# Optimization experiments

Hardware: AMD Instinct MI355X
Metric: run time of the kernel (lower is better)

## Reference

```python
import jax, jax.numpy as jnp
import numpy as np

N, M, D = 8192, 8192, 128

def setup_inputs() -> dict:
    key = jax.random.key(0)
    kq, kk, kv = jax.random.split(key, 3)
    Q = jax.random.normal(kq, (N, D), dtype=jnp.float32)
    K = jax.random.normal(kk, (M, D), dtype=jnp.float32)
    V = jax.random.normal(kv, (M, D), dtype=jnp.float32)
    return {"Q": Q, "K": K, "V": V}

def reference(Q, K, V):
    # scores: [N, M], unscaled QK^T
    scores = Q @ K.T
    # NOTE: original uses torch.softmax(scores, dim=0, dtype=float) -> softmax over the
    # QUERY axis (axis 0), normalizing each key-column across queries.
    attn = jax.nn.softmax(scores.astype(jnp.float32), axis=0)
    return attn @ V  # [N, D]
```

## Files before the change

### kernel.cpp

```cpp
#include <hip/hip_runtime.h>
#include <hip/hip_bf16.h>
#include <math.h>

constexpr int N = 8192, M = 8192, D = 128;
constexpr int NE = N * D;
constexpr float SHIFT = 60.0f;
constexpr float LOG2E = 1.4426950408889634f;
constexpr float S2 = 86.56170245333781f;
constexpr int SN_A = 16;
constexpr int PC_KS = 8;
constexpr int MK = M / 32;

typedef unsigned short u16;
typedef unsigned int u32;
using short8 = __attribute__((ext_vector_type(8))) short;
using f32x4  = __attribute__((ext_vector_type(4))) float;

#define MFMA16(a, b, c) __builtin_amdgcn_mfma_f32_16x16x32_bf16((a), (b), (c), 0, 0, 0)

#if __has_builtin(__builtin_amdgcn_exp2f)
#define EXP2(x) __builtin_amdgcn_exp2f(x)
#else
#define EXP2(x) __expf((x) * 0.6931471805599453f)
#endif

constexpr int PR = 40;
constexpr int CP = 136;
constexpr int KP = 136;
constexpr int WP = 72;
constexpr int PP = 72;

__device__ __forceinline__ u16 f2bf_rn(float x) {
  unsigned int u = __float_as_uint(x);
  return (u16)((u + 0x7fffu + ((u >> 16) & 1u)) >> 16);
}
__device__ __forceinline__ float bf2f(u16 h) { return __uint_as_float((unsigned)h << 16); }

__device__ __forceinline__ size_t qk_frag(int rowblk, int kblk, int lane) {
  return (((size_t)rowblk * 4 + kblk) * 64 + lane) * 8;
}
__device__ __forceinline__ size_t pw_frag(int blk16, int mkblk, int lane) {
  return (((size_t)blk16 * MK + mkblk) * 64 + lane) * 8;
}

__global__ __launch_bounds__(256) void convert_frag2(const float4* __restrict__ Qs,
                                                     const float4* __restrict__ Ks,
                                                     u16* __restrict__ Qhi, u16* __restrict__ Qlo,
                                                     u16* __restrict__ Khi, u16* __restrict__ Klo,
                                                     float* __restrict__ colsum) {
  __shared__ u16 LH[64 * CP];
  __shared__ u16 LL[64 * CP];
  const int tid = threadIdx.x;
  const bool isK = blockIdx.y != 0;
  const float4* src = isK ? Ks : Qs;
  u16* hi = isK ? Khi : Qhi;
  u16* lo = isK ? Klo : Qlo;
  const float sc = isK ? 1.0f : LOG2E;
  const int row0 = blockIdx.x * 64;

  if (blockIdx.x == 0 && !isK) {
#pragma unroll
    for (int k = 0; k < M / 256; ++k) colsum[tid + k * 256] = 0.f;
  }

#pragma unroll
  for (int it = 0; it < 8; ++it) {
    int idx = tid + it * 256;
    int rr = idx >> 5, g = idx & 31;
    float4 f = src[(size_t)(row0 + rr) * 32 + g];
    float v[4] = {f.x, f.y, f.z, f.w};
    u16 h[4], l4[4];
#pragma unroll
    for (int j = 0; j < 4; ++j) {
      float x = v[j] * sc;
      h[j] = f2bf_rn(x);
      l4[j] = f2bf_rn(x - bf2f(h[j]));
    }
    u32* ph = (u32*)(LH + rr * CP + g * 4);
    u32* pl = (u32*)(LL + rr * CP + g * 4);
    ph[0] = (u32)h[0] | ((u32)h[1] << 16);
    ph[1] = (u32)h[2] | ((u32)h[3] << 16);
    pl[0] = (u32)l4[0] | ((u32)l4[1] << 16);
    pl[1] = (u32)l4[2] | ((u32)l4[3] << 16);
  }
  __syncthreads();

#pragma unroll
  for (int it = 0; it < 4; ++it) {
    int idx = tid + it * 256;
    int tau = idx >> 6, l = idx & 63;
    int rowblk = tau >> 2, kblk = tau & 3;
    int d = kblk * 32 + (l >> 4) * 8;
    int nl;
    if (isK) {
      nl = ((rowblk >> 1) << 5) + ((l & 15) << 1) + (rowblk & 1);
    } else {
      nl = rowblk * 16 + (l & 15);
    }
    size_t off = qk_frag((row0 >> 4) + rowblk, kblk, l);
    *(short8*)(hi + off) = *(const short8*)(LH + nl * CP + d);
    *(short8*)(lo + off) = *(const short8*)(LL + nl * CP + d);
  }
}

__global__ __launch_bounds__(256, 4) void pass_a_frag(const u16* __restrict__ Qh,
                                                      const u16* __restrict__ Ql,
                                                      const u16* __restrict__ Kh,
                                                      const u16* __restrict__ Kl,
                                                      float* __restrict__ colsum,
                                                      u16* __restrict__ Pf) {
  __shared__ u16 PW[4][2][32 * PR];
  const int tid = threadIdx.x;
  const int w = tid >> 6, lane = tid & 63;
  const int r = lane & 15, q = lane >> 4;
  const int cbase = blockIdx.x * 128 + 32 * w;
  const int mymk = blockIdx.x * 4 + w;
  const int n0 = blockIdx.y * (N / SN_A);

  short8 kh[4][2], kl[4][2];
#pragma unroll
  for (int kk = 0; kk < 4; ++kk)
#pragma unroll
    for (int c = 0; c < 2; ++c) {
      size_t off = qk_frag((cbase >> 4) + c, kk, lane);
      kh[kk][c] = *(const short8*)(Kh + off);
      kl[kk][c] = *(const short8*)(Kl + off);
    }

  float csum[2] = {0.f, 0.f};

#pragma unroll 2
  for (int s = 0; s < (N / SN_A) / 32; ++s) {
    const int nb = n0 + s * 32;
    u16* pw = PW[w][s & 1];
    u32* pwD = (u32*)pw;

    f32x4 acc[2][2];
#pragma unroll
    for (int t = 0; t < 2; ++t)
#pragma unroll
      for (int c = 0; c < 2; ++c) acc[t][c] = (f32x4){-S2, -S2, -S2, -S2};

#pragma unroll
    for (int kk = 0; kk < 4; ++kk) {
      short8 ah[2], al[2];
#pragma unroll
      for (int t = 0; t < 2; ++t) {
        size_t off = qk_frag((nb >> 4) + t, kk, lane);
        ah[t] = *(const short8*)(Qh + off);
        al[t] = *(const short8*)(Ql + off);
      }
#pragma unroll
      for (int t = 0; t < 2; ++t)
#pragma unroll
        for (int c = 0; c < 2; ++c) {
          acc[t][c] = MFMA16(ah[t], kh[kk][c], acc[t][c]);
          acc[t][c] = MFMA16(al[t], kh[kk][c], acc[t][c]);
          acc[t][c] = MFMA16(ah[t], kl[kk][c], acc[t][c]);
        }
    }

#pragma unroll
    for (int t = 0; t < 2; ++t)
#pragma unroll
      for (int rg = 0; rg < 4; ++rg) {
        float e0 = EXP2(acc[t][0][rg]);
        float e1 = EXP2(acc[t][1][rg]);
        csum[0] += e0;
        csum[1] += e1;
        u32 pk = (u32)f2bf_rn(e0) | ((u32)f2bf_rn(e1) << 16);
        pwD[(16 * t + 4 * q + rg) * (PR / 2) + r] = pk;
      }
#pragma unroll
    for (int t = 0; t < 2; ++t) {
      short8 v = *(const short8*)(pw + (16 * t + r) * PR + q * 8);
      *(short8*)(Pf + pw_frag((nb >> 4) + t, mymk, lane)) = v;
    }
  }

  csum[0] += __shfl_xor(csum[0], 16);
  csum[0] += __shfl_xor(csum[0], 32);
  csum[1] += __shfl_xor(csum[1], 16);
  csum[1] += __shfl_xor(csum[1], 32);
  if (lane < 16) {
    atomicAdd(&colsum[cbase + 2 * lane], csum[0]);
    atomicAdd(&colsum[cbase + 2 * lane + 1], csum[1]);
  }
}

__global__ __launch_bounds__(256) void scale_transpose_frag(const float* __restrict__ V,
                                                            const float* __restrict__ colsum,
                                                            u16* __restrict__ Wf) {
  __shared__ float Vs[64][132];
  __shared__ float rls[64];
  const int tid = threadIdx.x;
  const int m0 = blockIdx.x * 64;
#pragma unroll
  for (int it = 0; it < 8; ++it) {
    int idx = tid + it * 256;
    int rr = idx >> 5, g = idx & 31;
    float4 v = *(const float4*)(V + (size_t)(m0 + rr) * D + g * 4);
    Vs[rr][g * 4 + 0] = v.x; Vs[rr][g * 4 + 1] = v.y;
    Vs[rr][g * 4 + 2] = v.z; Vs[rr][g * 4 + 3] = v.w;
  }
  if (tid < 64) rls[tid] = 1.0f / colsum[m0 + tid];
  __syncthreads();
#pragma unroll
  for (int it = 0; it < 4; ++it) {
    int idx = tid + it * 256;
    int dd = idx >> 3, g = idx & 7;
    short8 o;
#pragma unroll
    for (int j = 0; j < 8; ++j) {
      int mm = g * 8 + j;
      o[j] = (short)f2bf_rn(Vs[mm][dd] * rls[mm]);
    }
    *(short8*)(Wf + pw_frag(dd >> 4, (m0 >> 5) + (g >> 2), (dd & 15) + ((g & 3) << 4))) = o;
  }
}

template <bool ATOMIC>
__global__ __launch_bounds__(256, 4) void pass_c_kern(const u16* __restrict__ Pf,
                                                      const u16* __restrict__ Wf,
                                                      float* __restrict__ dst) {
  const int tid = threadIdx.x;
  const int w = tid >> 6, lane = tid & 63;
  const int r = lane & 15, q = lane >> 4;
  const int nblk0 = blockIdx.x * 8 + w * 2;
  const int mk0 = blockIdx.y * (MK / PC_KS);
  constexpr int CNT = MK / PC_KS;

  f32x4 acc[2][8];
#pragma unroll
  for (int i = 0; i < 2; ++i)
#pragma unroll
    for (int dt = 0; dt < 8; ++dt) acc[i][dt] = (f32x4){0.f, 0.f, 0.f, 0.f};

  short8 c0 = *(const short8*)(Pf + pw_frag(nblk0 + 0, mk0, lane));
  short8 c1 = *(const short8*)(Pf + pw_frag(nblk0 + 1, mk0, lane));
  short8 x0 = *(const short8*)(Pf + pw_frag(nblk0 + 0, mk0 + 1, lane));
  short8 x1 = *(const short8*)(Pf + pw_frag(nblk0 + 1, mk0 + 1, lane));

  for (int mk = 0; mk < CNT; ++mk) {
    const int mkg = mk0 + mk;
    const int mk2 = mk + 2 < CNT ? mkg + 2 : mk0;
    short8 p0 = *(const short8*)(Pf + pw_frag(nblk0 + 0, mk2, lane));
    short8 p1 = *(const short8*)(Pf + pw_frag(nblk0 + 1, mk2, lane));
#pragma unroll
    for (int dt = 0; dt < 8; ++dt) {
      short8 b = *(const short8*)(Wf + pw_frag(dt, mkg, lane));
      acc[0][dt] = MFMA16(c0, b, acc[0][dt]);
      acc[1][dt] = MFMA16(c1, b, acc[1][dt]);
    }
    c0 = x0; c1 = x1; x0 = p0; x1 = p1;
  }

  if (ATOMIC) {
#pragma unroll
    for (int i = 0; i < 2; ++i)
#pragma unroll
      for (int dt = 0; dt < 8; ++dt)
#pragma unroll
        for (int rg = 0; rg < 4; ++rg)
          atomicAdd(&dst[(size_t)((nblk0 + i) * 16 + q * 4 + rg) * D + dt * 16 + r],
                    acc[i][dt][rg]);
  } else {
    float* part = dst + (size_t)blockIdx.y * NE;
#pragma unroll
    for (int i = 0; i < 2; ++i)
#pragma unroll
      for (int dt = 0; dt < 8; ++dt)
#pragma unroll
        for (int rg = 0; rg < 4; ++rg)
          part[(size_t)((nblk0 + i) * 16 + q * 4 + rg) * D + dt * 16 + r] = acc[i][dt][rg];
  }
}

__global__ __launch_bounds__(256) void reduce_out(const float4* __restrict__ part,
                                                  float4* __restrict__ out) {
  int i = blockIdx.x * 256 + threadIdx.x;
  float4 s = part[i];
#pragma unroll
  for (int k = 1; k < PC_KS; ++k) {
    float4 p = part[(size_t)k * (NE / 4) + i];
    s.x += p.x; s.y += p.y; s.z += p.z; s.w += p.w;
  }
  out[i] = s;
}

__global__ __launch_bounds__(256) void convert_hilo2(const float4* __restrict__ Qs,
                                                     const float4* __restrict__ Ks,
                                                     ushort4* __restrict__ Qhi, ushort4* __restrict__ Qlo,
                                                     ushort4* __restrict__ Khi, ushort4* __restrict__ Klo) {
  int i = blockIdx.x * 256 + threadIdx.x;
  const float4* src = blockIdx.y ? Ks : Qs;
  ushort4* hi = blockIdx.y ? Khi : Qhi;
  ushort4* lo = blockIdx.y ? Klo : Qlo;
  float4 f = src[i];
  float v[4] = {f.x, f.y, f.z, f.w};
  u16 hs[4], ls[4];
#pragma unroll
  for (int j = 0; j < 4; ++j) {
    hs[j] = f2bf_rn(v[j]);
    ls[j] = f2bf_rn(v[j] - bf2f(hs[j]));
  }
  hi[i] = make_ushort4(hs[0], hs[1], hs[2], hs[3]);
  lo[i] = make_ushort4(ls[0], ls[1], ls[2], ls[3]);
}

__global__ __launch_bounds__(256, 4) void pass_a_fb(const u16* __restrict__ Qh,
                                                    const u16* __restrict__ Ql,
                                                    const u16* __restrict__ Kh,
                                                    const u16* __restrict__ Kl,
                                                    float* __restrict__ colsum) {
  const int tid = threadIdx.x;
  const int w = tid >> 6, lane = tid & 63;
  const int r = lane & 15, q = lane >> 4;
  const int cbase = blockIdx.x * 128 + 32 * w;
  const int n0 = blockIdx.y * (N / 16);

  short8 kh[4][2], kl[4][2];
#pragma unroll
  for (int kk = 0; kk < 4; ++kk)
#pragma unroll
    for (int c = 0; c < 2; ++c) {
      kh[kk][c] = *(const short8*)(Kh + (size_t)(cbase + 16 * c + r) * D + kk * 32 + q * 8);
      kl[kk][c] = *(const short8*)(Kl + (size_t)(cbase + 16 * c + r) * D + kk * 32 + q * 8);
    }

  float csum[2] = {0.f, 0.f};
  for (int s = 0; s < 16; ++s) {
    const int nb = n0 + s * 32;
    f32x4 acc[2][2];
#pragma unroll
    for (int t = 0; t < 2; ++t)
#pragma unroll
      for (int c = 0; c < 2; ++c) acc[t][c] = (f32x4){0.f, 0.f, 0.f, 0.f};
#pragma unroll
    for (int kk = 0; kk < 4; ++kk) {
      short8 ah[2], al[2];
#pragma unroll
      for (int t = 0; t < 2; ++t) {
        ah[t] = *(const short8*)(Qh + (size_t)(nb + t * 16 + r) * D + kk * 32 + q * 8);
        al[t] = *(const short8*)(Ql + (size_t)(nb + t * 16 + r) * D + kk * 32 + q * 8);
      }
#pragma unroll
      for (int t = 0; t < 2; ++t)
#pragma unroll
        for (int c = 0; c < 2; ++c) {
          acc[t][c] = MFMA16(ah[t], kh[kk][c], acc[t][c]);
          acc[t][c] = MFMA16(al[t], kh[kk][c], acc[t][c]);
          acc[t][c] = MFMA16(ah[t], kl[kk][c], acc[t][c]);
        }
    }
#pragma unroll
    for (int t = 0; t < 2; ++t)
#pragma unroll
      for (int c = 0; c < 2; ++c)
#pragma unroll
        for (int rg = 0; rg < 4; ++rg) csum[c] += __expf(acc[t][c][rg] - SHIFT);
  }
  csum[0] += __shfl_xor(csum[0], 16);
  csum[0] += __shfl_xor(csum[0], 32);
  csum[1] += __shfl_xor(csum[1], 16);
  csum[1] += __shfl_xor(csum[1], 32);
  if (lane < 16) {
    atomicAdd(&colsum[cbase + r], csum[0]);
    atomicAdd(&colsum[cbase + 16 + r], csum[1]);
  }
}

__global__ __launch_bounds__(256) void scale_transpose_fb(const float* __restrict__ V,
                                                          const float* __restrict__ colsum,
                                                          u16* __restrict__ Wt) {
  __shared__ float Vs[64][132];
  __shared__ float rls[64];
  const int tid = threadIdx.x;
  const int m0 = blockIdx.x * 64;
#pragma unroll
  for (int it = 0; it < 8; ++it) {
    int idx = tid + it * 256;
    int rr = idx >> 5, g = idx & 31;
    float4 v = *(const float4*)(V + (size_t)(m0 + rr) * D + g * 4);
    Vs[rr][g * 4 + 0] = v.x; Vs[rr][g * 4 + 1] = v.y;
    Vs[rr][g * 4 + 2] = v.z; Vs[rr][g * 4 + 3] = v.w;
  }
  if (tid < 64) rls[tid] = 1.0f / colsum[m0 + tid];
  __syncthreads();
#pragma unroll
  for (int it = 0; it < 4; ++it) {
    int idx = tid + it * 256;
    int dd = idx >> 3, g = idx & 7;
    short8 o;
#pragma unroll
    for (int j = 0; j < 8; ++j) {
      int mm = g * 8 + j;
      o[j] = (short)f2bf_rn(Vs[mm][dd] * rls[mm]);
    }
    *(short8*)(Wt + (size_t)dd * M + m0 + g * 8) = o;
  }
}

__global__ __launch_bounds__(256, 2) void pass_c_fb(const u16* __restrict__ Qh,
                                                    const u16* __restrict__ Ql,
                                                    const u16* __restrict__ Kh,
                                                    const u16* __restrict__ Kl,
                                                    const u16* __restrict__ Wt,
                                                    float* __restrict__ out) {
  __shared__ u16 KsH[64 * KP];
  __shared__ u16 KsL[64 * KP];
  __shared__ u16 Ws[128 * WP];
  __shared__ u16 Ps[4][16 * PP];
  const int tid = threadIdx.x;
  const int w = tid >> 6, lane = tid & 63;
  const int r = lane & 15, q = lane >> 4;
  const size_t nrow = (size_t)blockIdx.x * 64 + w * 16 + r;
  const int mbase = blockIdx.y * (M / 4);

  short8 qh[4], ql[4];
#pragma unroll
  for (int kk = 0; kk < 4; ++kk) {
    qh[kk] = *(const short8*)(Qh + nrow * D + kk * 32 + q * 8);
    ql[kk] = *(const short8*)(Ql + nrow * D + kk * 32 + q * 8);
  }

  f32x4 oacc[8];
#pragma unroll
  for (int dt = 0; dt < 8; ++dt) oacc[dt] = (f32x4){0.f, 0.f, 0.f, 0.f};

  for (int mt = 0; mt < (M / 4) / 64; ++mt) {
    const int m0 = mbase + mt * 64;
    __syncthreads();
#pragma unroll
    for (int it = 0; it < 4; ++it) {
      int idx = tid + it * 256;
      int rr = idx >> 4, g = idx & 15;
      *(short8*)(KsH + rr * KP + g * 8) = *(const short8*)(Kh + (size_t)(m0 + rr) * D + g * 8);
      *(short8*)(KsL + rr * KP + g * 8) = *(const short8*)(Kl + (size_t)(m0 + rr) * D + g * 8);
    }
#pragma unroll
    for (int it = 0; it < 4; ++it) {
      int idx = tid + it * 256;
      int dd = idx >> 3, g = idx & 7;
      *(short8*)(Ws + dd * WP + g * 8) = *(const short8*)(Wt + (size_t)dd * M + m0 + g * 8);
    }
    __syncthreads();

    f32x4 sacc[4];
#pragma unroll
    for (int t = 0; t < 4; ++t) sacc[t] = (f32x4){0.f, 0.f, 0.f, 0.f};
#pragma unroll
    for (int kk = 0; kk < 4; ++kk) {
      short8 bh[4], bl[4];
#pragma unroll
      for (int t = 0; t < 4; ++t) {
        bh[t] = *(const short8*)(KsH + (t * 16 + r) * KP + kk * 32 + q * 8);
        bl[t] = *(const short8*)(KsL + (t * 16 + r) * KP + kk * 32 + q * 8);
      }
#pragma unroll
      for (int t = 0; t < 4; ++t) {
        sacc[t] = MFMA16(qh[kk], bh[t], sacc[t]);
        sacc[t] = MFMA16(qh[kk], bl[t], sacc[t]);
        sacc[t] = MFMA16(ql[kk], bh[t], sacc[t]);
      }
    }
#pragma unroll
    for (int t = 0; t < 4; ++t)
#pragma unroll
      for (int rg = 0; rg < 4; ++rg)
        Ps[w][(q * 4 + rg) * PP + t * 16 + r] = f2bf_rn(__expf(sacc[t][rg] - SHIFT));
#pragma unroll
    for (int kk = 0; kk < 2; ++kk) {
      short8 pa = *(const short8*)(Ps[w] + r * PP + kk * 32 + q * 8);
#pragma unroll
      for (int dt = 0; dt < 8; ++dt) {
        short8 wb = *(const short8*)(Ws + (dt * 16 + r) * WP + kk * 32 + q * 8);
        oacc[dt] = MFMA16(pa, wb, oacc[dt]);
      }
    }
  }
#pragma unroll
  for (int dt = 0; dt < 8; ++dt)
#pragma unroll
    for (int rg = 0; rg < 4; ++rg)
      atomicAdd(&out[((size_t)blockIdx.x * 64 + w * 16 + q * 4 + rg) * D + dt * 16 + r],
                oacc[dt][rg]);
}

extern "C" void kernel_launch(void* const* d_in, const int* in_sizes, int n_in,
                              void* d_out, int out_size, void* d_ws, size_t ws_size,
                              hipStream_t stream) {
  const float* Q = (const float*)d_in[0];
  const float* K = (const float*)d_in[1];
  const float* V = (const float*)d_in[2];
  float* out = (float*)d_out;

  u16* Qh = (u16*)d_ws;
  u16* Ql = Qh + NE;
  u16* Kh = Ql + NE;
  u16* Kl = Kh + NE;
  u16* Wb = Kl + NE;
  float* colsum = (float*)(Wb + NE);
  u16* Pf = (u16*)(colsum + M);
  float* Opart = (float*)(Pf + (size_t)N * M);
  const size_t need_mat = (size_t)5 * NE * 2 + M * 4 + (size_t)N * M * 2;
  const size_t need_part = need_mat + (size_t)PC_KS * NE * 4;
  const bool mat = ws_size >= need_mat;
  const bool part = ws_size >= need_part;

  if (mat) {
    convert_frag2<<<dim3(N / 64, 2), 256, 0, stream>>>(
        (const float4*)Q, (const float4*)K, Qh, Ql, Kh, Kl, colsum);
    pass_a_frag<<<dim3(M / 128, SN_A), 256, 0, stream>>>(Qh, Ql, Kh, Kl, colsum, Pf);
    scale_transpose_frag<<<M / 64, 256, 0, stream>>>(V, colsum, Wb);
    if (part) {
      pass_c_kern<false><<<dim3(N / 128, PC_KS), 256, 0, stream>>>(Pf, Wb, Opart);
      reduce_out<<<NE / 4 / 256, 256, 0, stream>>>((const float4*)Opart, (float4*)out);
    } else {
      hipMemsetAsync(d_out, 0, (size_t)N * D * sizeof(float), stream);
      pass_c_kern<true><<<dim3(N / 128, PC_KS), 256, 0, stream>>>(Pf, Wb, out);
    }
  } else {
    hipMemsetAsync(colsum, 0, M * sizeof(float), stream);
    hipMemsetAsync(d_out, 0, (size_t)N * D * sizeof(float), stream);
    convert_hilo2<<<dim3(NE / 4 / 256, 2), 256, 0, stream>>>(
        (const float4*)Q, (const float4*)K, (ushort4*)Qh, (ushort4*)Ql, (ushort4*)Kh, (ushort4*)Kl);
    pass_a_fb<<<dim3(M / 128, 16), 256, 0, stream>>>(Qh, Ql, Kh, Kl, colsum);
    scale_transpose_fb<<<M / 64, 256, 0, stream>>>(V, colsum, Wb);
    pass_c_fb<<<dim3(N / 64, 4), 256, 0, stream>>>(Qh, Ql, Kh, Kl, Wb, out);
  }
}
```

Measured before the change: 173.0 us.

## Move P fragment transpose from pass A epilogue into pass C via LDS

```diff
diff --git a/kernel.cpp b/kernel.cpp
--- a/kernel.cpp
+++ b/kernel.cpp
@@ -15,6 +15,7 @@
 typedef unsigned int u32;
 using short8 = __attribute__((ext_vector_type(8))) short;
 using f32x4  = __attribute__((ext_vector_type(4))) float;
+using u32x4  = __attribute__((ext_vector_type(4))) unsigned int;
 
 #define MFMA16(a, b, c) __builtin_amdgcn_mfma_f32_16x16x32_bf16((a), (b), (c), 0, 0, 0)
 
@@ -109,7 +110,6 @@
                                                       const u16* __restrict__ Kl,
                                                       float* __restrict__ colsum,
                                                       u16* __restrict__ Pf) {
-  __shared__ u16 PW[4][2][32 * PR];
   const int tid = threadIdx.x;
   const int w = tid >> 6, lane = tid & 63;
   const int r = lane & 15, q = lane >> 4;
@@ -132,8 +132,6 @@
 #pragma unroll 2
   for (int s = 0; s < (N / SN_A) / 32; ++s) {
     const int nb = n0 + s * 32;
-    u16* pw = PW[w][s & 1];
-    u32* pwD = (u32*)pw;
 
     f32x4 acc[2][2];
 #pragma unroll
@@ -161,20 +159,17 @@
     }
 
 #pragma unroll
-    for (int t = 0; t < 2; ++t)
+    for (int t = 0; t < 2; ++t) {
+      u32x4 blob;
 #pragma unroll
       for (int rg = 0; rg < 4; ++rg) {
         float e0 = EXP2(acc[t][0][rg]);
         float e1 = EXP2(acc[t][1][rg]);
         csum[0] += e0;
         csum[1] += e1;
-        u32 pk = (u32)f2bf_rn(e0) | ((u32)f2bf_rn(e1) << 16);
-        pwD[(16 * t + 4 * q + rg) * (PR / 2) + r] = pk;
+        blob[rg] = (u32)f2bf_rn(e0) | ((u32)f2bf_rn(e1) << 16);
       }
-#pragma unroll
-    for (int t = 0; t < 2; ++t) {
-      short8 v = *(const short8*)(pw + (16 * t + r) * PR + q * 8);
-      *(short8*)(Pf + pw_frag((nb >> 4) + t, mymk, lane)) = v;
+      *(u32x4*)(Pf + pw_frag((nb >> 4) + t, mymk, lane)) = blob;
     }
   }
 
@@ -223,6 +218,7 @@
 __global__ __launch_bounds__(256, 4) void pass_c_kern(const u16* __restrict__ Pf,
                                                       const u16* __restrict__ Wf,
                                                       float* __restrict__ dst) {
+  __shared__ u32 T[4][2][2][16 * (PR / 2)];
   const int tid = threadIdx.x;
   const int w = tid >> 6, lane = tid & 63;
   const int r = lane & 15, q = lane >> 4;
@@ -236,23 +232,37 @@
 #pragma unroll
     for (int dt = 0; dt < 8; ++dt) acc[i][dt] = (f32x4){0.f, 0.f, 0.f, 0.f};
 
-  short8 c0 = *(const short8*)(Pf + pw_frag(nblk0 + 0, mk0, lane));
-  short8 c1 = *(const short8*)(Pf + pw_frag(nblk0 + 1, mk0, lane));
-  short8 x0 = *(const short8*)(Pf + pw_frag(nblk0 + 0, mk0 + 1, lane));
-  short8 x1 = *(const short8*)(Pf + pw_frag(nblk0 + 1, mk0 + 1, lane));
+  u32x4 bc0 = *(const u32x4*)(Pf + pw_frag(nblk0 + 0, mk0, lane));
+  u32x4 bc1 = *(const u32x4*)(Pf + pw_frag(nblk0 + 1, mk0, lane));
+  u32x4 bn0 = *(const u32x4*)(Pf + pw_frag(nblk0 + 0, mk0 + 1, lane));
+  u32x4 bn1 = *(const u32x4*)(Pf + pw_frag(nblk0 + 1, mk0 + 1, lane));
+#pragma unroll
+  for (int rg = 0; rg < 4; ++rg) {
+    T[w][0][0][(4 * q + rg) * (PR / 2) + r] = bc0[rg];
+    T[w][0][1][(4 * q + rg) * (PR / 2) + r] = bc1[rg];
+  }
 
   for (int mk = 0; mk < CNT; ++mk) {
+    const int p = mk & 1;
+    short8 a0 = *(const short8*)((const u16*)T[w][p][0] + r * PR + q * 8);
+    short8 a1 = *(const short8*)((const u16*)T[w][p][1] + r * PR + q * 8);
+    const int mk2 = mk + 2 < CNT ? mk0 + mk + 2 : mk0;
+    u32x4 bf0 = *(const u32x4*)(Pf + pw_frag(nblk0 + 0, mk2, lane));
+    u32x4 bf1 = *(const u32x4*)(Pf + pw_frag(nblk0 + 1, mk2, lane));
+#pragma unroll
+    for (int rg = 0; rg < 4; ++rg) {
+      T[w][p ^ 1][0][(4 * q + rg) * (PR / 2) + r] = bn0[rg];
+      T[w][p ^ 1][1][(4 * q + rg) * (PR / 2) + r] = bn1[rg];
+    }
     const int mkg = mk0 + mk;
-    const int mk2 = mk + 2 < CNT ? mkg + 2 : mk0;
-    short8 p0 = *(const short8*)(Pf + pw_frag(nblk0 + 0, mk2, lane));
-    short8 p1 = *(const short8*)(Pf + pw_frag(nblk0 + 1, mk2, lane));
 #pragma unroll
     for (int dt = 0; dt < 8; ++dt) {
       short8 b = *(const short8*)(Wf + pw_frag(dt, mkg, lane));
-      acc[0][dt] = MFMA16(c0, b, acc[0][dt]);
-      acc[1][dt] = MFMA16(c1, b, acc[1][dt]);
-    }
-    c0 = x0; c1 = x1; x0 = p0; x1 = p1;
+      acc[0][dt] = MFMA16(a0, b, acc[0][dt]);
+      acc[1][dt] = MFMA16(a1, b, acc[1][dt]);
+    }
+    bn0 = bf0;
+    bn1 = bf1;
   }
 
   if (ATOMIC) {
```

Result: faster. 168.1 us (-2.8%).
